# Performance work log

Hardware: AMD Instinct MI355X
Metric: run time of the kernel (lower is better)

## Reference

```python
import jax, jax.numpy as jnp
import numpy as np

N_NODES = 100000
N_EDGES = 1600000
DIMS = [1, 20, 40, 60, 80, 100]  # int(k/5*qubo_size) for qubo_size=100


def setup_inputs() -> dict:
    key = jax.random.key(0)
    ks = jax.random.split(key, 16)
    inp = {
        "x": jax.random.normal(ks[0], (N_NODES, 1), dtype=jnp.float32),
        "edge_index": jax.random.randint(ks[1], (2, N_EDGES), 0, N_NODES, dtype=jnp.int64),
        "edge_weights": jax.random.uniform(ks[2], (N_EDGES,), dtype=jnp.float32),
    }
    for i in range(5):
        fan_in, fan_out = DIMS[i], DIMS[i + 1]
        scale = (2.0 / (fan_in + fan_out)) ** 0.5  # glorot-ish
        inp[f"W{i+1}"] = jax.random.normal(ks[3 + 2 * i], (fan_in, fan_out), dtype=jnp.float32) * scale
        inp[f"b{i+1}"] = jnp.zeros((fan_out,), dtype=jnp.float32)
    return inp


def reference(x, edge_index, edge_weights, W1, b1, W2, b2, W3, b3, W4, b4, W5, b5):
    n = x.shape[0]
    src, dst = edge_index[0], edge_index[1]
    # GCN symmetric normalization with self loops (fill value 1.0)
    deg = jax.ops.segment_sum(edge_weights, dst, num_segments=n) + 1.0
    dinv = jnp.where(deg > 0, deg ** -0.5, 0.0)
    norm = dinv[src] * edge_weights * dinv[dst]  # [E]
    self_norm = dinv * dinv                      # [N], self-loop weight 1

    def gcn_layer(h, W, b):
        h = h @ W  # [N, out]
        agg = jax.ops.segment_sum(h[src] * norm[:, None], dst, num_segments=n)
        agg = agg + h * self_norm[:, None]
        return agg + b

    for W, b in ((W1, b1), (W2, b2), (W3, b3), (W4, b4), (W5, b5)):
        x = gcn_layer(x, W, b)
    return jax.nn.relu(x)
```

## Files before the change

### kernel.cpp

```cpp
#include <hip/hip_runtime.h>


#define TBB 1024
#define TBK 512
#define BN 256
#define NBLK 256
#define STAGE 4096
#define CAP 4864
#define MAGIC 0x13572468

__device__ __forceinline__ void chains_block(
    const float* __restrict__ W1, const float* __restrict__ b1,
    const float* __restrict__ W2, const float* __restrict__ b2,
    const float* __restrict__ W3, const float* __restrict__ b3,
    const float* __restrict__ W4, const float* __restrict__ b4,
    const float* __restrict__ W5, float* __restrict__ coef,
    int* lflag, float (*A)[112], float (*Bm)[112]) {
    int t = threadIdx.x;
    if (t < 20) { A[0][t] = W1[t]; A[1][t] = b1[t]; }
    __syncthreads();
    if (t < 40) {
        for (int c = 0; c < 2; ++c) {
            float acc = 0.f;
            for (int k = 0; k < 20; ++k) acc += A[c][k] * W2[k * 40 + t];
            Bm[c][t] = acc;
        }
        Bm[2][t] = b2[t];
    }
    __syncthreads();
    if (t < 60) {
        for (int c = 0; c < 3; ++c) {
            float acc = 0.f;
            for (int k = 0; k < 40; ++k) acc += Bm[c][k] * W3[k * 60 + t];
            A[c][t] = acc;
        }
        A[3][t] = b3[t];
    }
    __syncthreads();
    if (t < 80) {
        for (int c = 0; c < 4; ++c) {
            float acc = 0.f;
            for (int k = 0; k < 60; ++k) acc += A[c][k] * W4[k * 80 + t];
            Bm[c][t] = acc;
        }
        Bm[4][t] = b4[t];
    }
    __syncthreads();
    if (t < 100) {
        int nz = 0;
        for (int c = 0; c < 5; ++c) {
            float acc = 0.f;
            for (int k = 0; k < 80; ++k) acc += Bm[c][k] * W5[k * 100 + t];
            coef[c * 100 + t] = acc;
            if (c > 0 && acc != 0.0f) nz = 1;
        }
        if (nz) atomicOr(lflag, 1);
    }
}

__global__ __launch_bounds__(TBB) void k_build(const int* __restrict__ src,
                                               const int* __restrict__ dst,
                                               const float* __restrict__ w,
                                               int* __restrict__ gcur,
                                               int* __restrict__ ready,
                                               int2* __restrict__ payload,
                                               const float* __restrict__ W1, const float* __restrict__ b1,
                                               const float* __restrict__ W2, const float* __restrict__ b2,
                                               const float* __restrict__ W3, const float* __restrict__ b3,
                                               const float* __restrict__ W4, const float* __restrict__ b4,
                                               const float* __restrict__ W5, float* __restrict__ coef,
                                               int* __restrict__ uflag,
                                               int E, int B, int chunk) {
    __shared__ int lcur[512];
    __shared__ int lbase[512];
    __shared__ int goff[512];
    __shared__ int2 staged[STAGE];
    __shared__ unsigned short jbuf[STAGE];
    int blk = blockIdx.x, tid = threadIdx.x;
    if (blk == NBLK) {
        float (*A)[112]  = (float (*)[112])staged;
        float (*Bm)[112] = (float (*)[112])((char*)staged + 5 * 112 * 4);
        if (tid == 0) lcur[0] = 0;
        __syncthreads();
        chains_block(W1, b1, W2, b2, W3, b3, W4, b4, W5, coef, &lcur[0], A, Bm);
        __syncthreads();
        if (tid == 0) uflag[0] = lcur[0] ? 0 : 1;
        return;
    }
    if (blk == 0) {
        for (int j2 = tid; j2 < B; j2 += TBB) gcur[j2] = 0;
        __syncthreads();
        if (tid == 0)
            __hip_atomic_store(ready, MAGIC, __ATOMIC_RELEASE, __HIP_MEMORY_SCOPE_AGENT);
    }
    bool waited = (blk == 0);
    int e0 = blk * chunk, e1 = min(E, e0 + chunk);
    for (int sbeg = e0; sbeg < e1; sbeg += STAGE) {
        int send = min(e1, sbeg + STAGE);
        int cnt = send - sbeg;
        if (tid < 512) lcur[tid] = 0;
        __syncthreads();
        int es[4], ed[4]; float ew[4]; int ne = 0;
        for (int i = sbeg + tid; i < send; i += TBB) {
            es[ne] = src[i]; ed[ne] = dst[i]; ew[ne] = w[i]; ++ne;
        }
        for (int k = 0; k < ne; ++k) atomicAdd(&lcur[ed[k] >> 8], 1);
        __syncthreads();
        int myv = (tid < 512) ? lcur[tid] : 0;
        if (!waited) {
            if (tid == 0) {
                while (__hip_atomic_load(ready, __ATOMIC_ACQUIRE, __HIP_MEMORY_SCOPE_AGENT) != MAGIC)
                    __builtin_amdgcn_s_sleep(1);
            }
            __syncthreads();
            waited = true;
        }
        if (tid < B && myv > 0)
            goff[tid] = atomicAdd(&gcur[tid], myv);
        if (tid < 512) lbase[tid] = myv;
        __syncthreads();
        for (int o = 1; o < 512; o <<= 1) {
            int t = (tid >= o && tid < 512) ? lbase[tid - o] : 0;
            __syncthreads();
            if (tid < 512) lbase[tid] += t;
            __syncthreads();
        }
        if (tid < 512) {
            int ex = lbase[tid] - myv;
            lbase[tid] = ex;
            lcur[tid] = ex;
        }
        __syncthreads();
        for (int k = 0; k < ne; ++k) {
            int j = ed[k] >> 8;
            int p = atomicAdd(&lcur[j], 1);
            staged[p] = make_int2(es[k] | ((ed[k] & 255) << 17), __float_as_int(ew[k]));
            jbuf[p] = (unsigned short)j;
        }
        __syncthreads();
        for (int p = tid; p < cnt; p += TBB) {
            int j = jbuf[p];
            int slot = goff[j] + (p - lbase[j]);
            if (slot < CAP) payload[(size_t)j * CAP + slot] = staged[p];
        }
        __syncthreads();
    }
}

__global__ __launch_bounds__(TBK) void k_bstats(const int* __restrict__ gcur,
                                                const int2* __restrict__ payload,
                                                const float* __restrict__ x,
                                                float* __restrict__ dinv,
                                                float* __restrict__ selfn,
                                                float* __restrict__ qx0,
                                                float* __restrict__ qy0, int n) {
    __shared__ float wdeg[BN];
    int j = blockIdx.x;
    int tid = threadIdx.x;
    if (tid < BN) wdeg[tid] = 0.f;
    __syncthreads();
    int len = min(gcur[j], CAP);
    const int2* row = payload + (size_t)j * CAP;
    const int4* row4 = (const int4*)row;
    int len2 = len >> 1;
    for (int i = tid; i < len2; i += TBK) {
        int4 p = row4[i];
        atomicAdd(&wdeg[(p.x >> 17) & 255], __int_as_float(p.y));
        atomicAdd(&wdeg[(p.z >> 17) & 255], __int_as_float(p.w));
    }
    if (tid == 0 && (len & 1)) {
        int2 p = row[len - 1];
        atomicAdd(&wdeg[(p.x >> 17) & 255], __int_as_float(p.y));
    }
    __syncthreads();
    if (tid < BN) {
        int v = j * BN + tid;
        if (v < n) {
            float di = rsqrtf(wdeg[tid] + 1.0f);
            dinv[v] = di;
            selfn[v] = di * di;
            qx0[v] = di * x[v];
            qy0[v] = di;
        }
    }
}

__global__ __launch_bounds__(TBK) void k_mid(const int* __restrict__ gcur,
                                             const int2* __restrict__ payload,
                                             const float* __restrict__ qxin,
                                             const float* __restrict__ qyin,
                                             const float* __restrict__ selfn,
                                             const int* __restrict__ uflag,
                                             float* __restrict__ qxout,
                                             float* __restrict__ qyout, int n) {
    __shared__ float sacc_x[BN];
    __shared__ float sacc_y[BN];
    int j = blockIdx.x;
    int tid = threadIdx.x;
    if (tid < BN) { sacc_x[tid] = 0.f; sacc_y[tid] = 0.f; }
    __syncthreads();
    const int skipy = uflag[0];
    int len = min(gcur[j], CAP);
    const int2* row = payload + (size_t)j * CAP;
    const int4* row4 = (const int4*)row;
    int len2 = len >> 1;
    for (int i = tid; i < len2; i += TBK) {
        int4 p = row4[i];
        int s1 = p.x & 0x1FFFF, s2 = p.z & 0x1FFFF;
        int ld1 = (p.x >> 17) & 255, ld2 = (p.z >> 17) & 255;
        float w1 = __int_as_float(p.y), w2 = __int_as_float(p.w);
        if (skipy) {
            float qx1 = qxin[s1], qx2 = qxin[s2];
            atomicAdd(&sacc_x[ld1], w1 * qx1);
            atomicAdd(&sacc_x[ld2], w2 * qx2);
        } else {
            float qx1 = qxin[s1], qy1 = qyin[s1];
            float qx2 = qxin[s2], qy2 = qyin[s2];
            atomicAdd(&sacc_x[ld1], w1 * qx1);
            atomicAdd(&sacc_y[ld1], w1 * qy1);
            atomicAdd(&sacc_x[ld2], w2 * qx2);
            atomicAdd(&sacc_y[ld2], w2 * qy2);
        }
    }
    if (tid == 0 && (len & 1)) {
        int2 p = row[len - 1];
        int s = p.x & 0x1FFFF, ld = (p.x >> 17) & 255;
        float wv = __int_as_float(p.y);
        atomicAdd(&sacc_x[ld], wv * qxin[s]);
        if (!skipy) atomicAdd(&sacc_y[ld], wv * qyin[s]);
    }
    __syncthreads();
    if (tid < BN) {
        int v = j * BN + tid;
        if (v < n) {
            float sf = selfn[v];
            qxout[v] = sf * (sacc_x[tid] + qxin[v]);
            if (!skipy) qyout[v] = sf * (sacc_y[tid] + qyin[v]);
        }
    }
}

__global__ __launch_bounds__(TBK) void k_last(const int* __restrict__ gcur,
                                              const int2* __restrict__ payload,
                                              const float* __restrict__ qx4,
                                              const float* __restrict__ qy1,
                                              const float* __restrict__ qy2,
                                              const float* __restrict__ qy3,
                                              const float* __restrict__ qy4,
                                              const float* __restrict__ dinv,
                                              const int* __restrict__ uflag,
                                              const float* __restrict__ coef,
                                              const float* __restrict__ b5,
                                              float4* __restrict__ out, int n) {
    __shared__ float sacc_x[BN];
    __shared__ float scoef[500];
    __shared__ float sb5[100];
    __shared__ float snode[BN * 5];
    int j = blockIdx.x;
    int tid = threadIdx.x;
    if (tid < BN) sacc_x[tid] = 0.f;
    for (int i = tid; i < 500; i += TBK) scoef[i] = coef[i];
    for (int i = tid; i < 100; i += TBK) sb5[i] = b5[i];
    __syncthreads();
    const int skipy = uflag[0];
    int len = min(gcur[j], CAP);
    const int2* row = payload + (size_t)j * CAP;
    const int4* row4 = (const int4*)row;
    int len2 = len >> 1;
    for (int i = tid; i < len2; i += TBK) {
        int4 p = row4[i];
        float qx1 = qx4[p.x & 0x1FFFF];
        float qx2 = qx4[p.z & 0x1FFFF];
        atomicAdd(&sacc_x[(p.x >> 17) & 255], __int_as_float(p.y) * qx1);
        atomicAdd(&sacc_x[(p.z >> 17) & 255], __int_as_float(p.w) * qx2);
    }
    if (tid == 0 && (len & 1)) {
        int2 p = row[len - 1];
        atomicAdd(&sacc_x[(p.x >> 17) & 255], __int_as_float(p.y) * qx4[p.x & 0x1FFFF]);
    }
    __syncthreads();
    if (tid < BN) {
        int v = j * BN + tid;
        if (v < n) {
            float dv = dinv[v];
            float inv = 1.0f / dv;
            snode[tid * 5 + 0] = dv * (sacc_x[tid] + qx4[v]);
            snode[tid * 5 + 1] = skipy ? 0.f : qy4[v] * inv;
            snode[tid * 5 + 2] = skipy ? 0.f : qy3[v] * inv;
            snode[tid * 5 + 3] = skipy ? 0.f : qy2[v] * inv;
            snode[tid * 5 + 4] = skipy ? 0.f : qy1[v] * inv;
        }
    }
    __syncthreads();
    int base_v = j * BN;
    int nv = min(BN, n - base_v);
    int total4 = nv * 25;
    for (int q = tid; q < total4; q += TBK) {
        int lv = q / 25;
        int col4 = q - lv * 25;
        int c0 = col4 * 4;
        float a5 = snode[lv * 5 + 0], u4 = snode[lv * 5 + 1], u3 = snode[lv * 5 + 2],
              u2 = snode[lv * 5 + 3], u1 = snode[lv * 5 + 4];
        float4 r;
        float* rp = (float*)&r;
#pragma unroll
        for (int kk = 0; kk < 4; ++kk) {
            int c = c0 + kk;
            rp[kk] = fmaxf(sb5[c] + a5 * scoef[c] + u4 * scoef[100 + c] + u3 * scoef[200 + c]
                           + u2 * scoef[300 + c] + u1 * scoef[400 + c], 0.f);
        }
        out[(size_t)(base_v + lv) * 25 + col4] = r;
    }
}


extern "C" void kernel_launch(void* const* d_in, const int* in_sizes, int n_in,
                              void* d_out, int out_size, void* d_ws, size_t ws_size,
                              hipStream_t stream) {
    const float* x  = (const float*)d_in[0];
    const int*   ei = (const int*)d_in[1];
    const float* w  = (const float*)d_in[2];
    const float* W1 = (const float*)d_in[3];  const float* b1 = (const float*)d_in[4];
    const float* W2 = (const float*)d_in[5];  const float* b2 = (const float*)d_in[6];
    const float* W3 = (const float*)d_in[7];  const float* b3 = (const float*)d_in[8];
    const float* W4 = (const float*)d_in[9];  const float* b4 = (const float*)d_in[10];
    const float* W5 = (const float*)d_in[11]; const float* b5 = (const float*)d_in[12];

    const int n = in_sizes[0];
    const int E = in_sizes[2];
    const int* src = ei;
    const int* dst = ei + E;

    const int B = (n + BN - 1) / BN;
    const int chunk = (E + NBLK - 1) / NBLK;

    char* ws = (char*)d_ws;
    size_t off = 0;
    auto alloc = [&](size_t bytes) -> void* {
        void* p = ws + off;
        off += (bytes + 255) & ~(size_t)255;
        return p;
    };
    int*   gcur    = (int*)alloc((size_t)B * 4);
    int*   ready   = (int*)alloc(256);
    int*   uflag   = (int*)alloc(256);
    float* dinv    = (float*)alloc((size_t)n * 4);
    float* selfn   = (float*)alloc((size_t)n * 4);
    float* coef    = (float*)alloc(512 * 4);
    int2*  payload = (int2*)alloc((size_t)B * CAP * 8);
    float* qx[5];
    float* qy[5];
    for (int i = 0; i < 5; ++i) qx[i] = (float*)alloc((size_t)n * 4);
    for (int i = 0; i < 5; ++i) qy[i] = (float*)alloc((size_t)n * 4);

    k_build<<<NBLK + 1, TBB, 0, stream>>>(src, dst, w, gcur, ready, payload,
                                          W1, b1, W2, b2, W3, b3, W4, b4, W5, coef,
                                          uflag, E, B, chunk);
    k_bstats<<<B, TBK, 0, stream>>>(gcur, payload, x, dinv, selfn, qx[0], qy[0], n);

    for (int k = 1; k < 5; ++k)
        k_mid<<<B, TBK, 0, stream>>>(gcur, payload, qx[k - 1], qy[k - 1], selfn, uflag,
                                     qx[k], qy[k], n);
    k_last<<<B, TBK, 0, stream>>>(gcur, payload, qx[4], qy[1], qy[2], qy[3], qy[4],
                                  dinv, uflag, coef, b5, (float4*)d_out, n);
}
```

Baseline: 203.7 us.

## Fuse degree into build, split bucket aggregation across blocks with global atomics

Weighted degree accumulation moves into the build kernel as global atomics on a per-node array, which removes the separate pass that re-read the payload for degrees. Each propagation step now splits every destination bucket's edge list across three smaller blocks. The partial sums are combined with global atomicAdd into output buffers that are zeroed beforehand. The last layer is split into a gather kernel and a separate epilogue kernel. This raises block count and occupancy for the gather, at the cost of extra global atomics, zeroing traffic and one more launch.

```diff
diff --git a/kernel.cpp b/kernel.cpp
--- a/kernel.cpp
+++ b/kernel.cpp
@@ -3,10 +3,12 @@
 
 #define TBB 1024
 #define TBK 512
+#define TBM 256
 #define BN 256
 #define NBLK 256
 #define STAGE 4096
 #define CAP 4864
+#define FSPLIT 3
 #define MAGIC 0x13572468
 
 __device__ __forceinline__ void chains_block(
@@ -64,13 +66,14 @@
                                                int* __restrict__ gcur,
                                                int* __restrict__ ready,
                                                int2* __restrict__ payload,
+                                               float* __restrict__ wdeg,
                                                const float* __restrict__ W1, const float* __restrict__ b1,
                                                const float* __restrict__ W2, const float* __restrict__ b2,
                                                const float* __restrict__ W3, const float* __restrict__ b3,
                                                const float* __restrict__ W4, const float* __restrict__ b4,
                                                const float* __restrict__ W5, float* __restrict__ coef,
                                                int* __restrict__ uflag,
-                                               int E, int B, int chunk) {
+                                               int E, int B, int chunk, int n) {
     __shared__ int lcur[512];
     __shared__ int lbase[512];
     __shared__ int goff[512];
@@ -89,6 +92,11 @@
     }
     if (blk == 0) {
         for (int j2 = tid; j2 < B; j2 += TBB) gcur[j2] = 0;
+        float4* w4 = (float4*)wdeg;
+        int nq = n >> 2;
+        float4 z4 = make_float4(0.f, 0.f, 0.f, 0.f);
+        for (int i = tid; i < nq; i += TBB) w4[i] = z4;
+        for (int i = (nq << 2) + tid; i < n; i += TBB) wdeg[i] = 0.f;
         __syncthreads();
         if (tid == 0)
             __hip_atomic_store(ready, MAGIC, __ATOMIC_RELEASE, __HIP_MEMORY_SCOPE_AGENT);
@@ -140,52 +148,38 @@
         __syncthreads();
         for (int p = tid; p < cnt; p += TBB) {
             int j = jbuf[p];
+            int2 e = staged[p];
             int slot = goff[j] + (p - lbase[j]);
-            if (slot < CAP) payload[(size_t)j * CAP + slot] = staged[p];
-        }
-        __syncthreads();
-    }
-}
-
-__global__ __launch_bounds__(TBK) void k_bstats(const int* __restrict__ gcur,
-                                                const int2* __restrict__ payload,
-                                                const float* __restrict__ x,
-                                                float* __restrict__ dinv,
-                                                float* __restrict__ selfn,
-                                                float* __restrict__ qx0,
-                                                float* __restrict__ qy0, int n) {
-    __shared__ float wdeg[BN];
-    int j = blockIdx.x;
+            if (slot < CAP) payload[(size_t)j * CAP + slot] = e;
+            atomicAdd(&wdeg[j * BN + ((e.x >> 17) & 255)], __int_as_float(e.y));
+        }
+        __syncthreads();
+    }
+}
+
+__global__ __launch_bounds__(TBM) void k_bstats2(const float* __restrict__ wdeg,
+                                                 const float* __restrict__ x,
+                                                 float* __restrict__ dinv,
+                                                 float* __restrict__ selfn,
+                                                 float* __restrict__ qx0,
+                                                 float* __restrict__ qy0,
+                                                 float4* __restrict__ zbase,
+                                                 int zcount, int n) {
     int tid = threadIdx.x;
-    if (tid < BN) wdeg[tid] = 0.f;
-    __syncthreads();
-    int len = min(gcur[j], CAP);
-    const int2* row = payload + (size_t)j * CAP;
-    const int4* row4 = (const int4*)row;
-    int len2 = len >> 1;
-    for (int i = tid; i < len2; i += TBK) {
-        int4 p = row4[i];
-        atomicAdd(&wdeg[(p.x >> 17) & 255], __int_as_float(p.y));
-        atomicAdd(&wdeg[(p.z >> 17) & 255], __int_as_float(p.w));
-    }
-    if (tid == 0 && (len & 1)) {
-        int2 p = row[len - 1];
-        atomicAdd(&wdeg[(p.x >> 17) & 255], __int_as_float(p.y));
-    }
-    __syncthreads();
-    if (tid < BN) {
-        int v = j * BN + tid;
-        if (v < n) {
-            float di = rsqrtf(wdeg[tid] + 1.0f);
-            dinv[v] = di;
-            selfn[v] = di * di;
-            qx0[v] = di * x[v];
-            qy0[v] = di;
-        }
-    }
-}
-
-__global__ __launch_bounds__(TBK) void k_mid(const int* __restrict__ gcur,
+    int gt = blockIdx.x * TBM + tid;
+    int stride = gridDim.x * TBM;
+    float4 z4 = make_float4(0.f, 0.f, 0.f, 0.f);
+    for (int i = gt; i < zcount; i += stride) zbase[i] = z4;
+    if (gt < n) {
+        float di = rsqrtf(wdeg[gt] + 1.0f);
+        dinv[gt] = di;
+        selfn[gt] = di * di;
+        qx0[gt] = di * x[gt];
+        qy0[gt] = di;
+    }
+}
+
+__global__ __launch_bounds__(TBM) void k_mid(const int* __restrict__ gcur,
                                              const int2* __restrict__ payload,
                                              const float* __restrict__ qxin,
                                              const float* __restrict__ qyin,
@@ -193,98 +187,112 @@
                                              const int* __restrict__ uflag,
                                              float* __restrict__ qxout,
                                              float* __restrict__ qyout, int n) {
-    __shared__ float sacc_x[BN];
-    __shared__ float sacc_y[BN];
-    int j = blockIdx.x;
+    __shared__ float sx[BN];
+    __shared__ float sy[BN];
+    int bid = blockIdx.x;
+    int j = bid / FSPLIT, h = bid - j * FSPLIT;
     int tid = threadIdx.x;
-    if (tid < BN) { sacc_x[tid] = 0.f; sacc_y[tid] = 0.f; }
-    __syncthreads();
     const int skipy = uflag[0];
+    int v = j * BN + tid;
+    if (h == 0 && v < n) {
+        sx[tid] = qxin[v];
+        sy[tid] = skipy ? 0.f : qyin[v];
+    } else {
+        sx[tid] = 0.f;
+        sy[tid] = 0.f;
+    }
+    __syncthreads();
     int len = min(gcur[j], CAP);
     const int2* row = payload + (size_t)j * CAP;
     const int4* row4 = (const int4*)row;
     int len2 = len >> 1;
-    for (int i = tid; i < len2; i += TBK) {
+    int r0 = h * len2 / FSPLIT, r1 = (h + 1) * len2 / FSPLIT;
+    for (int i = r0 + tid; i < r1; i += TBM) {
         int4 p = row4[i];
-        int s1 = p.x & 0x1FFFF, s2 = p.z & 0x1FFFF;
+        int sa = p.x & 0x1FFFF, sb = p.z & 0x1FFFF;
         int ld1 = (p.x >> 17) & 255, ld2 = (p.z >> 17) & 255;
         float w1 = __int_as_float(p.y), w2 = __int_as_float(p.w);
         if (skipy) {
-            float qx1 = qxin[s1], qx2 = qxin[s2];
-            atomicAdd(&sacc_x[ld1], w1 * qx1);
-            atomicAdd(&sacc_x[ld2], w2 * qx2);
+            atomicAdd(&sx[ld1], w1 * qxin[sa]);
+            atomicAdd(&sx[ld2], w2 * qxin[sb]);
         } else {
-            float qx1 = qxin[s1], qy1 = qyin[s1];
-            float qx2 = qxin[s2], qy2 = qyin[s2];
-            atomicAdd(&sacc_x[ld1], w1 * qx1);
-            atomicAdd(&sacc_y[ld1], w1 * qy1);
-            atomicAdd(&sacc_x[ld2], w2 * qx2);
-            atomicAdd(&sacc_y[ld2], w2 * qy2);
-        }
-    }
-    if (tid == 0 && (len & 1)) {
+            atomicAdd(&sx[ld1], w1 * qxin[sa]);
+            atomicAdd(&sy[ld1], w1 * qyin[sa]);
+            atomicAdd(&sx[ld2], w2 * qxin[sb]);
+            atomicAdd(&sy[ld2], w2 * qyin[sb]);
+        }
+    }
+    if (h == 0 && tid == 0 && (len & 1)) {
         int2 p = row[len - 1];
         int s = p.x & 0x1FFFF, ld = (p.x >> 17) & 255;
         float wv = __int_as_float(p.y);
-        atomicAdd(&sacc_x[ld], wv * qxin[s]);
-        if (!skipy) atomicAdd(&sacc_y[ld], wv * qyin[s]);
-    }
-    __syncthreads();
-    if (tid < BN) {
-        int v = j * BN + tid;
-        if (v < n) {
-            float sf = selfn[v];
-            qxout[v] = sf * (sacc_x[tid] + qxin[v]);
-            if (!skipy) qyout[v] = sf * (sacc_y[tid] + qyin[v]);
-        }
-    }
-}
-
-__global__ __launch_bounds__(TBK) void k_last(const int* __restrict__ gcur,
-                                              const int2* __restrict__ payload,
-                                              const float* __restrict__ qx4,
-                                              const float* __restrict__ qy1,
-                                              const float* __restrict__ qy2,
-                                              const float* __restrict__ qy3,
-                                              const float* __restrict__ qy4,
-                                              const float* __restrict__ dinv,
-                                              const int* __restrict__ uflag,
-                                              const float* __restrict__ coef,
-                                              const float* __restrict__ b5,
-                                              float4* __restrict__ out, int n) {
-    __shared__ float sacc_x[BN];
+        atomicAdd(&sx[ld], wv * qxin[s]);
+        if (!skipy) atomicAdd(&sy[ld], wv * qyin[s]);
+    }
+    __syncthreads();
+    if (v < n) {
+        float sf = selfn[v];
+        atomicAdd(&qxout[v], sf * sx[tid]);
+        if (!skipy) atomicAdd(&qyout[v], sf * sy[tid]);
+    }
+}
+
+__global__ __launch_bounds__(TBM) void k_lastg(const int* __restrict__ gcur,
+                                               const int2* __restrict__ payload,
+                                               const float* __restrict__ qx4,
+                                               const float* __restrict__ dinv,
+                                               float* __restrict__ a5b, int n) {
+    __shared__ float sx[BN];
+    int bid = blockIdx.x;
+    int j = bid / FSPLIT, h = bid - j * FSPLIT;
+    int tid = threadIdx.x;
+    int v = j * BN + tid;
+    sx[tid] = (h == 0 && v < n) ? qx4[v] : 0.f;
+    __syncthreads();
+    int len = min(gcur[j], CAP);
+    const int2* row = payload + (size_t)j * CAP;
+    const int4* row4 = (const int4*)row;
+    int len2 = len >> 1;
+    int r0 = h * len2 / FSPLIT, r1 = (h + 1) * len2 / FSPLIT;
+    for (int i = r0 + tid; i < r1; i += TBM) {
+        int4 p = row4[i];
+        float q1 = qx4[p.x & 0x1FFFF];
+        float q2 = qx4[p.z & 0x1FFFF];
+        atomicAdd(&sx[(p.x >> 17) & 255], __int_as_float(p.y) * q1);
+        atomicAdd(&sx[(p.z >> 17) & 255], __int_as_float(p.w) * q2);
+    }
+    if (h == 0 && tid == 0 && (len & 1)) {
+        int2 p = row[len - 1];
+        atomicAdd(&sx[(p.x >> 17) & 255], __int_as_float(p.y) * qx4[p.x & 0x1FFFF]);
+    }
+    __syncthreads();
+    if (v < n) atomicAdd(&a5b[v], dinv[v] * sx[tid]);
+}
+
+__global__ __launch_bounds__(TBK) void k_epi(const float* __restrict__ a5b,
+                                             const float* __restrict__ qy1,
+                                             const float* __restrict__ qy2,
+                                             const float* __restrict__ qy3,
+                                             const float* __restrict__ qy4,
+                                             const float* __restrict__ dinv,
+                                             const int* __restrict__ uflag,
+                                             const float* __restrict__ coef,
+                                             const float* __restrict__ b5,
+                                             float4* __restrict__ out, int n) {
     __shared__ float scoef[500];
     __shared__ float sb5[100];
     __shared__ float snode[BN * 5];
     int j = blockIdx.x;
     int tid = threadIdx.x;
-    if (tid < BN) sacc_x[tid] = 0.f;
     for (int i = tid; i < 500; i += TBK) scoef[i] = coef[i];
     for (int i = tid; i < 100; i += TBK) sb5[i] = b5[i];
-    __syncthreads();
     const int skipy = uflag[0];
-    int len = min(gcur[j], CAP);
-    const int2* row = payload + (size_t)j * CAP;
-    const int4* row4 = (const int4*)row;
-    int len2 = len >> 1;
-    for (int i = tid; i < len2; i += TBK) {
-        int4 p = row4[i];
-        float qx1 = qx4[p.x & 0x1FFFF];
-        float qx2 = qx4[p.z & 0x1FFFF];
-        atomicAdd(&sacc_x[(p.x >> 17) & 255], __int_as_float(p.y) * qx1);
-        atomicAdd(&sacc_x[(p.z >> 17) & 255], __int_as_float(p.w) * qx2);
-    }
-    if (tid == 0 && (len & 1)) {
-        int2 p = row[len - 1];
-        atomicAdd(&sacc_x[(p.x >> 17) & 255], __int_as_float(p.y) * qx4[p.x & 0x1FFFF]);
-    }
-    __syncthreads();
     if (tid < BN) {
         int v = j * BN + tid;
         if (v < n) {
             float dv = dinv[v];
             float inv = 1.0f / dv;
-            snode[tid * 5 + 0] = dv * (sacc_x[tid] + qx4[v]);
+            snode[tid * 5 + 0] = a5b[v];
             snode[tid * 5 + 1] = skipy ? 0.f : qy4[v] * inv;
             snode[tid * 5 + 2] = skipy ? 0.f : qy3[v] * inv;
             snode[tid * 5 + 3] = skipy ? 0.f : qy2[v] * inv;
@@ -346,21 +354,30 @@
     int*   uflag   = (int*)alloc(256);
     float* dinv    = (float*)alloc((size_t)n * 4);
     float* selfn   = (float*)alloc((size_t)n * 4);
+    float* wdeg    = (float*)alloc((size_t)n * 4);
     float* coef    = (float*)alloc(512 * 4);
     int2*  payload = (int2*)alloc((size_t)B * CAP * 8);
+    size_t nr = ((size_t)n * 4 + 255) & ~(size_t)255;
+    char*  zbase = (char*)alloc(nr * 9);
     float* qx[5];
     float* qy[5];
-    for (int i = 0; i < 5; ++i) qx[i] = (float*)alloc((size_t)n * 4);
-    for (int i = 0; i < 5; ++i) qy[i] = (float*)alloc((size_t)n * 4);
-
-    k_build<<<NBLK + 1, TBB, 0, stream>>>(src, dst, w, gcur, ready, payload,
+    qx[0] = (float*)alloc((size_t)n * 4);
+    qy[0] = (float*)alloc((size_t)n * 4);
+    for (int i = 1; i < 5; ++i) qx[i] = (float*)(zbase + (size_t)(i - 1) * nr);
+    for (int i = 1; i < 5; ++i) qy[i] = (float*)(zbase + (size_t)(3 + i) * nr);
+    float* a5b = (float*)(zbase + 8 * nr);
+    const int zcount = (int)(nr * 9 / 16);
+
+    k_build<<<NBLK + 1, TBB, 0, stream>>>(src, dst, w, gcur, ready, payload, wdeg,
                                           W1, b1, W2, b2, W3, b3, W4, b4, W5, coef,
-                                          uflag, E, B, chunk);
-    k_bstats<<<B, TBK, 0, stream>>>(gcur, payload, x, dinv, selfn, qx[0], qy[0], n);
+                                          uflag, E, B, chunk, n);
+    k_bstats2<<<B, TBM, 0, stream>>>(wdeg, x, dinv, selfn, qx[0], qy[0],
+                                     (float4*)zbase, zcount, n);
 
     for (int k = 1; k < 5; ++k)
-        k_mid<<<B, TBK, 0, stream>>>(gcur, payload, qx[k - 1], qy[k - 1], selfn, uflag,
-                                     qx[k], qy[k], n);
-    k_last<<<B, TBK, 0, stream>>>(gcur, payload, qx[4], qy[1], qy[2], qy[3], qy[4],
-                                  dinv, uflag, coef, b5, (float4*)d_out, n);
-}
+        k_mid<<<B * FSPLIT, TBM, 0, stream>>>(gcur, payload, qx[k - 1], qy[k - 1], selfn,
+                                              uflag, qx[k], qy[k], n);
+    k_lastg<<<B * FSPLIT, TBM, 0, stream>>>(gcur, payload, qx[4], dinv, a5b, n);
+    k_epi<<<B, TBK, 0, stream>>>(a5b, qy[1], qy[2], qy[3], qy[4], dinv, uflag, coef, b5,
+                                 (float4*)d_out, n);
+}
```

Result: slower. 254.4 us (+24.9%).

## Bucket whole edge chunk in registers and scatter directly without LDS staging

Applied to the files above, without the earlier changes.

The build kernel now loads each block's entire edge chunk into registers (up to 7 edges per thread), counts per-bucket, reserves global offsets once, and writes each edge straight to its payload slot using a per-bucket LDS rank counter. This removes the staged LDS buffer, the 512-wide prefix scan and the multiple stage iterations and barriers. The cost is that global writes are no longer grouped by bucket, so they may be less coalesced, and the larger register arrays raise register pressure. It also assumes chunk is at most 7*1024 edges per block.

```diff
diff --git a/kernel.cpp b/kernel.cpp
--- a/kernel.cpp
+++ b/kernel.cpp
@@ -5,8 +5,8 @@
 #define TBK 512
 #define BN 256
 #define NBLK 256
-#define STAGE 4096
 #define CAP 4864
+#define EPB 7
 #define MAGIC 0x13572468
 
 __device__ __forceinline__ void chains_block(
@@ -71,20 +71,18 @@
                                                const float* __restrict__ W5, float* __restrict__ coef,
                                                int* __restrict__ uflag,
                                                int E, int B, int chunk) {
-    __shared__ int lcur[512];
-    __shared__ int lbase[512];
+    __shared__ int lcnt[512];
+    __shared__ int lrnk[512];
     __shared__ int goff[512];
-    __shared__ int2 staged[STAGE];
-    __shared__ unsigned short jbuf[STAGE];
+    __shared__ float chain_scratch[10][112];
     int blk = blockIdx.x, tid = threadIdx.x;
     if (blk == NBLK) {
-        float (*A)[112]  = (float (*)[112])staged;
-        float (*Bm)[112] = (float (*)[112])((char*)staged + 5 * 112 * 4);
-        if (tid == 0) lcur[0] = 0;
+        if (tid == 0) lcnt[0] = 0;
         __syncthreads();
-        chains_block(W1, b1, W2, b2, W3, b3, W4, b4, W5, coef, &lcur[0], A, Bm);
+        chains_block(W1, b1, W2, b2, W3, b3, W4, b4, W5, coef, &lcnt[0],
+                     &chain_scratch[0], &chain_scratch[5]);
         __syncthreads();
-        if (tid == 0) uflag[0] = lcur[0] ? 0 : 1;
+        if (tid == 0) uflag[0] = lcnt[0] ? 0 : 1;
         return;
     }
     if (blk == 0) {
@@ -93,57 +91,34 @@
         if (tid == 0)
             __hip_atomic_store(ready, MAGIC, __ATOMIC_RELEASE, __HIP_MEMORY_SCOPE_AGENT);
     }
-    bool waited = (blk == 0);
+    if (tid < 512) { lcnt[tid] = 0; lrnk[tid] = 0; }
+    __syncthreads();
     int e0 = blk * chunk, e1 = min(E, e0 + chunk);
-    for (int sbeg = e0; sbeg < e1; sbeg += STAGE) {
-        int send = min(e1, sbeg + STAGE);
-        int cnt = send - sbeg;
-        if (tid < 512) lcur[tid] = 0;
+    int es[EPB], ed[EPB]; float ew[EPB]; int ne = 0;
+    for (int i = e0 + tid; i < e1; i += TBB) {
+        es[ne] = src[i]; ed[ne] = dst[i]; ew[ne] = w[i]; ++ne;
+    }
+    for (int k = 0; k < ne; ++k) atomicAdd(&lcnt[ed[k] >> 8], 1);
+    __syncthreads();
+    if (blk != 0) {
+        if (tid == 0) {
+            while (__hip_atomic_load(ready, __ATOMIC_ACQUIRE, __HIP_MEMORY_SCOPE_AGENT) != MAGIC)
+                __builtin_amdgcn_s_sleep(1);
+        }
         __syncthreads();
-        int es[4], ed[4]; float ew[4]; int ne = 0;
-        for (int i = sbeg + tid; i < send; i += TBB) {
-            es[ne] = src[i]; ed[ne] = dst[i]; ew[ne] = w[i]; ++ne;
-        }
-        for (int k = 0; k < ne; ++k) atomicAdd(&lcur[ed[k] >> 8], 1);
-        __syncthreads();
-        int myv = (tid < 512) ? lcur[tid] : 0;
-        if (!waited) {
-            if (tid == 0) {
-                while (__hip_atomic_load(ready, __ATOMIC_ACQUIRE, __HIP_MEMORY_SCOPE_AGENT) != MAGIC)
-                    __builtin_amdgcn_s_sleep(1);
-            }
-            __syncthreads();
-            waited = true;
-        }
-        if (tid < B && myv > 0)
-            goff[tid] = atomicAdd(&gcur[tid], myv);
-        if (tid < 512) lbase[tid] = myv;
-        __syncthreads();
-        for (int o = 1; o < 512; o <<= 1) {
-            int t = (tid >= o && tid < 512) ? lbase[tid - o] : 0;
-            __syncthreads();
-            if (tid < 512) lbase[tid] += t;
-            __syncthreads();
-        }
-        if (tid < 512) {
-            int ex = lbase[tid] - myv;
-            lbase[tid] = ex;
-            lcur[tid] = ex;
-        }
-        __syncthreads();
-        for (int k = 0; k < ne; ++k) {
-            int j = ed[k] >> 8;
-            int p = atomicAdd(&lcur[j], 1);
-            staged[p] = make_int2(es[k] | ((ed[k] & 255) << 17), __float_as_int(ew[k]));
-            jbuf[p] = (unsigned short)j;
-        }
-        __syncthreads();
-        for (int p = tid; p < cnt; p += TBB) {
-            int j = jbuf[p];
-            int slot = goff[j] + (p - lbase[j]);
-            if (slot < CAP) payload[(size_t)j * CAP + slot] = staged[p];
-        }
-        __syncthreads();
+    }
+    if (tid < 512) {
+        int c = lcnt[tid];
+        if (c > 0) goff[tid] = atomicAdd(&gcur[tid], c);
+    }
+    __syncthreads();
+    for (int k = 0; k < ne; ++k) {
+        int j = ed[k] >> 8;
+        int r = atomicAdd(&lrnk[j], 1);
+        int slot = goff[j] + r;
+        if (slot < CAP)
+            payload[(size_t)j * CAP + slot] =
+                make_int2(es[k] | ((ed[k] & 255) << 17), __float_as_int(ew[k]));
     }
 }
 
```

After: 206.1 us. About the same (+1.2%).
